# Performance work log

Measured on AMD Instinct MI355X. Metric: run time of the kernel, lower is better.

Reference implementation:

```python
import jax, jax.numpy as jnp
import numpy as np

BS, HW, HIDDEN, TOK, NTOK = 32, 1024, 256, 768, 2048


def setup_inputs() -> dict:
    key = jax.random.key(0)
    ks = jax.random.split(key, 6)
    s = 0.02  # init scale for weights
    return {
        "src": jax.random.normal(ks[0], (HW, BS, HIDDEN), jnp.float32),
        "codebook": jax.random.normal(ks[1], (NTOK, TOK), jnp.float32),
        "w_head": jax.random.normal(ks[2], (TOK, HIDDEN), jnp.float32) * s,
        "w_tail": jax.random.normal(ks[3], (HIDDEN, TOK), jnp.float32) * s,
        "w_pos": jax.random.normal(ks[4], (TOK, TOK), jnp.float32) * s,
        "b_pos": jnp.zeros((TOK,), jnp.float32),
        "w_gate": jax.random.normal(ks[5], (2, 2 * TOK), jnp.float32) * s,
        "h": 32,
        "w": 32,
    }


def reference(src, codebook, w_head, w_tail, w_pos, b_pos, w_gate, h, w):
    N, bs, hidden = src.shape  # [num_visu_token, bs, hidden_dim]
    tok = codebook.shape[1]
    # permute(1,2,0).view(bs,-1,h,w)
    x = jnp.transpose(src, (1, 2, 0)).reshape(bs, hidden, h, w)
    # conv_head: 1x1 conv, no bias
    xq = jnp.einsum("bchw,oc->bohw", x, w_head)  # [bs, tok, h, w]
    # raw-memory reshape, matches torch .view(-1, token_dim)
    flat = xq.reshape(-1, tok)  # [bs*h*w, tok]
    d = (
        jnp.sum(flat * flat, axis=1, keepdims=True)
        - 2.0 * flat @ codebook.T
        + jnp.sum(codebook * codebook, axis=1)[None, :]
    )
    indices = jnp.argmin(d, axis=1)  # [bs*h*w]
    quantized = codebook[indices]  # gather
    # straight-through estimator
    quantized = flat + jax.lax.stop_gradient(quantized - flat)
    # pos_align linear
    quantized = quantized @ w_pos.T + b_pos
    # view(bs, N, tok).permute(0,2,1).view(bs,-1,h,w)
    emb = jnp.transpose(quantized.reshape(bs, N, tok), (0, 2, 1)).reshape(bs, tok, h, w)
    # gated fusion
    gate_in = jnp.concatenate([emb, xq], axis=1)  # [bs, 2*tok, h, w]
    scores = jax.nn.softmax(jnp.einsum("bchw,oc->bohw", gate_in, w_gate), axis=1)
    fused = emb * scores[:, 0:1] + xq * scores[:, 1:2]
    # conv_tail 1x1, then flatten(2).permute(2,0,1)
    out = jnp.einsum("bchw,oc->bohw", fused, w_tail)  # [bs, hidden, h, w]
    out = jnp.transpose(out.reshape(bs, hidden, -1), (2, 0, 1))  # [h*w, bs, hidden]
    return out, indices
```

## Files before the change

### kernel.cpp

```cpp
#include <hip/hip_runtime.h>
#include <cstdint>

#define BSZ 32
#define NVIS 1024
#define HID 256
#define TOKD 768
#define NCODE 2048
#define NPIX 32768

typedef unsigned short u16;
typedef _Float16 half8 __attribute__((ext_vector_type(8)));
typedef unsigned short ushort8 __attribute__((ext_vector_type(8)));
using f32x4 = __attribute__((ext_vector_type(4))) float;

#define AS1 __attribute__((address_space(1)))
#define AS3 __attribute__((address_space(3)))

__device__ __forceinline__ f32x4 mfmaF16(half8 a, half8 b, f32x4 c) {
  return __builtin_amdgcn_mfma_f32_16x16x32_f16(a, b, c, 0, 0, 0);
}

__device__ __forceinline__ unsigned long long pack_key(float d, int idx) {
  unsigned int b = __float_as_uint(d);
  b = (b & 0x80000000u) ? ~b : (b | 0x80000000u);
  return ((unsigned long long)b << 32) | (unsigned int)idx;
}

__device__ __forceinline__ void split16(float v, u16& h, u16& l) {
  union { _Float16 f; u16 u; } a, b;
  a.f = (_Float16)v;
  float hf = (float)a.f;
  b.f = (_Float16)(v - hf);
  h = a.u; l = b.u;
}

__global__ __launch_bounds__(256)
void prep1(const float* __restrict__ cb, const float* __restrict__ wh,
           const float* __restrict__ wt, const float* __restrict__ wp,
           const float* __restrict__ wg, const float* __restrict__ bp,
           u16* __restrict__ cbh, u16* __restrict__ cbl,
           u16* __restrict__ whh, u16* __restrict__ whl,
           float* __restrict__ cbn, float* __restrict__ Mm, float* __restrict__ uv,
           float* __restrict__ Gt, float* __restrict__ g2,
           float* __restrict__ ct0, float* __restrict__ cg) {
  const int bid = blockIdx.x, tid = threadIdx.x;
  if (bid < 6144) {
    int i = bid*256 + tid;
    u16 h, l; split16(cb[i], h, l);
    cbh[i] = h; cbl[i] = l;
  } else if (bid < 6912) {
    int i = (bid - 6144)*256 + tid;
    u16 h, l; split16(wh[i], h, l);
    whh[i] = h; whl[i] = l;
  } else if (bid < 7424) {
    int n = (bid - 6912)*4 + (tid >> 6);
    int lane = tid & 63;
    float a = 0.f;
#pragma unroll
    for (int i = 0; i < 12; ++i) { float v = cb[(long)n*TOKD + lane + 64*i]; a += v*v; }
#pragma unroll
    for (int off = 32; off; off >>= 1) a += __shfl_down(a, off);
    if (lane == 0) cbn[n] = a;
  } else if (bid < 7680) {
    int c2 = bid - 7424, c1 = tid;
    float acc = 0.f;
    for (int t = 0; t < TOKD; ++t) acc += wh[t*HID + c1] * wt[(long)c2*TOKD + t];
    Mm[c1*HID + c2] = acc;
  } else if (bid < 7682) {
    int o = bid - 7680, c1 = tid;
    float acc = 0.f;
    for (int t = 0; t < TOKD; ++t) acc += wh[t*HID + c1] * wg[o*(2*TOKD) + TOKD + t];
    uv[o*HID + c1] = acc;
  } else if (bid < 8450) {
    int rbid = bid - 7682;
    int c = rbid & 255, part = rbid >> 8;
    int tp = part*256 + tid;
    float acc = 0.f;
    for (int t = 0; t < TOKD; ++t) acc += wt[(long)c*TOKD + t] * wp[(long)t*TOKD + tp];
    Gt[(long)tp*HID + c] = acc;
  } else if (bid < 8453) {
    int tp = (bid - 8450)*256 + tid;
    float a0 = 0.f, a1 = 0.f;
    for (int t = 0; t < TOKD; ++t) {
      float wv = wp[(long)t*TOKD + tp];
      a0 += wv * wg[t];
      a1 += wv * wg[2*TOKD + t];
    }
    g2[tp] = a0; g2[TOKD + tp] = a1;
  } else if (bid < 8454) {
    int c = tid;
    float a = 0.f;
    for (int t = 0; t < TOKD; ++t) a += bp[t] * wt[(long)c*TOKD + t];
    ct0[c] = a;
  } else {
    int o = tid >> 6, lane = tid & 63;
    if (o < 2) {
      float a = 0.f;
      for (int t = lane; t < TOKD; t += 64) a += bp[t] * wg[o*(2*TOKD) + t];
#pragma unroll
      for (int off = 32; off; off >>= 1) a += __shfl_down(a, off);
      if (lane == 0) cg[o] = a;
    }
  }
}

__global__ __launch_bounds__(256)
void prep2(const float* __restrict__ cb, const float* __restrict__ Gt,
           const float* __restrict__ ct0, const float* __restrict__ g2,
           const float* __restrict__ cg, float* __restrict__ tc,
           float* __restrict__ gA) {
  __shared__ float cbs[8][TOKD];
  const int n0 = blockIdx.x * 8, tid = threadIdx.x;
  for (int i = tid; i < 8*TOKD; i += 256) cbs[i / TOKD][i % TOKD] = cb[(long)n0*TOKD + i];
  __syncthreads();
  float acc[8] = {};
  for (int t = 0; t < TOKD; ++t) {
    float gv = Gt[(long)t*HID + tid];
#pragma unroll
    for (int i = 0; i < 8; ++i) acc[i] += cbs[i][t] * gv;
  }
  float c0v = ct0[tid];
#pragma unroll
  for (int i = 0; i < 8; ++i) tc[(long)(n0+i)*HID + tid] = acc[i] + c0v;
  {
    int i = tid >> 5, l32 = tid & 31;
    float a0 = 0.f, a1 = 0.f;
    for (int t = l32; t < TOKD; t += 32) {
      float cv = cbs[i][t];
      a0 += cv * g2[t];
      a1 += cv * g2[TOKD + t];
    }
#pragma unroll
    for (int off = 16; off; off >>= 1) { a0 += __shfl_down(a0, off); a1 += __shfl_down(a1, off); }
    if (l32 == 0) { gA[n0+i] = a0 + cg[0]; gA[NCODE + n0+i] = a1 + cg[1]; }
  }
}

__global__ __launch_bounds__(256)
void head_mfma(const u16* __restrict__ whh, const u16* __restrict__ whl,
               const float* __restrict__ src,
               u16* __restrict__ xqh, u16* __restrict__ xql) {
  __shared__ u16 SM[32768] __attribute__((aligned(16)));
  u16* Ah = SM;
  u16* Al = SM + 8192;
  u16* Bh = SM + 16384;
  u16* Bl = SM + 24576;
  const int tid = threadIdx.x, lane = tid & 63, w = tid >> 6;
  const int n = lane & 15, q = lane >> 4;
  const int rh = w & 1, ch = w >> 1;
  const int obase = blockIdx.x * 128, pbase = blockIdx.y * 128, b = blockIdx.z;

  auto stageA = [&](int kc, int buf) {
#pragma unroll
    for (int is = 0; is < 2; ++is) {
      int c = is*256 + tid;
      int t = c >> 6, qq = (c >> 4) & 3, nn = c & 15;
      long off = (long)(obase + t*16 + nn)*HID + kc*32 + qq*8;
      __builtin_amdgcn_global_load_lds((AS1 void*)(whh + off),
          (AS3 void*)&Ah[buf*4096 + c*8], 16, 0, 0);
      __builtin_amdgcn_global_load_lds((AS1 void*)(whl + off),
          (AS3 void*)&Al[buf*4096 + c*8], 16, 0, 0);
    }
  };
  auto stageB = [&](int kc, int buf) {
#pragma unroll
    for (int is = 0; is < 2; ++is) {
      int c = is*256 + tid;
      int t = c >> 6, qq = (c >> 4) & 3, nn = c & 15;
      const float* gp = src + ((long)(pbase + t*16 + nn)*BSZ + b)*HID + kc*32 + qq*8;
      float4 v0 = *(const float4*)gp;
      float4 v1 = *(const float4*)(gp + 4);
      float vv[8] = {v0.x, v0.y, v0.z, v0.w, v1.x, v1.y, v1.z, v1.w};
      ushort8 hv, lv;
#pragma unroll
      for (int j = 0; j < 8; ++j) { u16 hs, ls; split16(vv[j], hs, ls); hv[j] = hs; lv[j] = ls; }
      *(ushort8*)&Bh[buf*4096 + c*8] = hv;
      *(ushort8*)&Bl[buf*4096 + c*8] = lv;
    }
  };

  f32x4 acc[4][4];
#pragma unroll
  for (int i = 0; i < 4; ++i)
#pragma unroll
    for (int j = 0; j < 4; ++j) acc[i][j] = (f32x4){0.f, 0.f, 0.f, 0.f};

  stageA(0, 0); stageB(0, 0);
  __syncthreads();

  for (int kt = 0; kt < HID/32; ++kt) {
    const int buf = kt & 1;
    if (kt + 1 < HID/32) { stageA(kt + 1, buf ^ 1); stageB(kt + 1, buf ^ 1); }
    half8 af[4][2], bf[4][2];
#pragma unroll
    for (int rt = 0; rt < 4; ++rt) {
      int idx = buf*4096 + ((rh*4 + rt)*64 + q*16 + n)*8;
      af[rt][0] = *(const half8*)&Ah[idx];
      af[rt][1] = *(const half8*)&Al[idx];
    }
#pragma unroll
    for (int ct = 0; ct < 4; ++ct) {
      int idx = buf*4096 + ((ch*4 + ct)*64 + q*16 + n)*8;
      bf[ct][0] = *(const half8*)&Bh[idx];
      bf[ct][1] = *(const half8*)&Bl[idx];
    }
#pragma unroll
    for (int rt = 0; rt < 4; ++rt)
#pragma unroll
      for (int ct = 0; ct < 4; ++ct) {
        acc[rt][ct] = mfmaF16(af[rt][0], bf[ct][0], acc[rt][ct]);
        acc[rt][ct] = mfmaF16(af[rt][0], bf[ct][1], acc[rt][ct]);
        acc[rt][ct] = mfmaF16(af[rt][1], bf[ct][0], acc[rt][ct]);
      }
    __syncthreads();
  }

#pragma unroll
  for (int pass = 0; pass < 2; ++pass) {
    u16* dst = pass ? xql : xqh;
#pragma unroll
    for (int rt = 0; rt < 4; ++rt)
#pragma unroll
      for (int ct = 0; ct < 4; ++ct)
#pragma unroll
        for (int reg = 0; reg < 4; ++reg) {
          u16 hs, ls; split16(acc[rt][ct][reg], hs, ls);
          int ol = rh*64 + rt*16 + q*4 + reg;
          int pl = ch*64 + ct*16 + n;
          SM[ol*136 + pl] = pass ? ls : hs;
        }
    __syncthreads();
#pragma unroll
    for (int s = 0; s < 8; ++s) {
      int cc = tid*8 + s;
      int o = cc >> 4, p8 = cc & 15;
      ushort8 v = *(const ushort8*)&SM[o*136 + p8*8];
      *(ushort8*)(dst + ((long)b*TOKD + obase + o)*NVIS + pbase + p8*8) = v;
    }
    __syncthreads();
  }
}

__global__ __launch_bounds__(256)
void retile(u16* __restrict__ bufH, u16* __restrict__ bufL) {
  __shared__ u16 T[96*136] __attribute__((aligned(16)));
  const long tile = blockIdx.x;
  const int tid = threadIdx.x;
#pragma unroll
  for (int pass = 0; pass < 2; ++pass) {
    u16* buf = pass ? bufL : bufH;
    if (pass) __syncthreads();
#pragma unroll
    for (int i = 0; i < 6; ++i) {
      int g = i*256 + tid;
      int row = g / 96, c16 = g % 96;
      ushort8 v = *(const ushort8*)(buf + tile*12288 + row*768 + c16*8);
      *(ushort8*)&T[c16*136 + row*8] = v;
    }
    __syncthreads();
#pragma unroll
    for (int i = 0; i < 6; ++i) {
      int g = i*256 + tid;
      int kc = g >> 6, lp = g & 63;
      int q = lp >> 4, n = lp & 15;
      ushort8 v = *(const ushort8*)&T[(kc*4 + q)*136 + n*8];
      *(ushort8*)(buf + tile*12288 + (long)kc*512 + lp*8) = v;
    }
  }
}

__global__ __launch_bounds__(512, 2)
void vq_mfma(const u16* __restrict__ xqh, const u16* __restrict__ xql,
             const u16* __restrict__ cbh, const u16* __restrict__ cbl,
             const float* __restrict__ cbn, unsigned long long* __restrict__ keys) {
  __shared__ u16 SM[65536] __attribute__((aligned(16)));
  const int bid = blockIdx.x;
  const int rowBlk = bid >> 3, codeBlk = bid & 7;
  const int rowTile0 = rowBlk * 16, codeTile0 = codeBlk * 16;
  const int tid = threadIdx.x, lane = tid & 63, w = tid >> 6;
  const int n = lane & 15, q = lane >> 4;
  const int wr = w >> 2, wc = w & 3;

  const size_t aOff = (size_t)(rowTile0 + 2*w) * 12288 + lane*8;
  const size_t bOff = (size_t)(codeTile0 + 2*w) * 12288 + lane*8;
  const int ldsChunk = (2*w)*512 + lane*8;

  auto STAGE = [&](int ht, int buf) {
    const int seg = (ht >= 48) ? 2 : ((ht >= 24) ? 1 : 0);
    const int kk = ht - seg * 24;
    const u16* pa = ((seg == 1) ? xql : xqh) + aOff + kk*512;
    const u16* pb = ((seg == 2) ? cbl : cbh) + bOff + kk*512;
    u16* la = &SM[buf*8192 + ldsChunk];
    u16* lb = &SM[32768 + buf*8192 + ldsChunk];
    __builtin_amdgcn_global_load_lds((AS1 void*)pa,           (AS3 void*)la,        16, 0, 0);
    __builtin_amdgcn_global_load_lds((AS1 void*)(pa + 12288), (AS3 void*)(la + 512), 16, 0, 0);
    __builtin_amdgcn_global_load_lds((AS1 void*)pb,           (AS3 void*)lb,        16, 0, 0);
    __builtin_amdgcn_global_load_lds((AS1 void*)(pb + 12288), (AS3 void*)(lb + 512), 16, 0, 0);
  };

  f32x4 acc[8][4];
#pragma unroll
  for (int a = 0; a < 8; ++a)
#pragma unroll
    for (int b2 = 0; b2 < 4; ++b2) acc[a][b2] = (f32x4){0.f, 0.f, 0.f, 0.f};

  STAGE(0, 0); STAGE(1, 1); STAGE(2, 2);

#pragma unroll 4
  for (int ht = 0; ht < 72; ++ht) {
    const int pf = (ht + 3 > 71) ? 71 : ht + 3;
    STAGE(pf, (ht + 3) & 3);
    asm volatile("s_waitcnt vmcnt(12)" ::: "memory");
    asm volatile("s_barrier" ::: "memory");
    const int abase = (ht & 3)*8192 + (wr*8)*512 + lane*8;
    const int bbase = 32768 + (ht & 3)*8192 + (wc*4)*512 + lane*8;
    half8 Af[8], Bf[4];
#pragma unroll
    for (int rt = 0; rt < 8; ++rt) Af[rt] = *(const half8*)&SM[abase + rt*512];
#pragma unroll
    for (int ct = 0; ct < 4; ++ct) Bf[ct] = *(const half8*)&SM[bbase + ct*512];
    asm volatile("s_waitcnt lgkmcnt(0)" ::: "memory");
    asm volatile("s_barrier" ::: "memory");
    __builtin_amdgcn_s_setprio(1);
#pragma unroll
    for (int rt = 0; rt < 8; ++rt)
#pragma unroll
      for (int ct = 0; ct < 4; ++ct)
        acc[rt][ct] = mfmaF16(Af[rt], Bf[ct], acc[rt][ct]);
    __builtin_amdgcn_s_setprio(0);
  }

  float cbv[4];
#pragma unroll
  for (int ct = 0; ct < 4; ++ct) cbv[ct] = cbn[(codeTile0 + wc*4 + ct)*16 + n];
#pragma unroll
  for (int rt = 0; rt < 8; ++rt) {
#pragma unroll
    for (int reg = 0; reg < 4; ++reg) {
      float bd = 3.4e38f; int bi = 0;
#pragma unroll
      for (int ct = 0; ct < 4; ++ct) {
        float d = cbv[ct] - 2.0f * acc[rt][ct][reg];
        int code = (codeTile0 + wc*4 + ct)*16 + n;
        if (d < bd) { bd = d; bi = code; }
      }
      unsigned long long k = pack_key(bd, bi);
      unsigned long long v;
      v = __shfl_xor(k, 1); k = (v < k) ? v : k;
      v = __shfl_xor(k, 2); k = (v < k) ? v : k;
      v = __shfl_xor(k, 4); k = (v < k) ? v : k;
      v = __shfl_xor(k, 8); k = (v < k) ? v : k;
      if (n == 0) {
        int row = (rowTile0 + wr*8 + rt)*16 + q*4 + reg;
        atomicMin(&keys[row], k);
      }
    }
  }
}

__global__ __launch_bounds__(256)
void fuse_out(const float* __restrict__ src, const unsigned long long* __restrict__ keys,
              const float* __restrict__ gA, const float* __restrict__ uvec,
              const float* __restrict__ Mm, const float* __restrict__ tailcode,
              float* __restrict__ out, float* __restrict__ outIdx) {
  __shared__ float ss[32][257];
  __shared__ float s0s[32];
  __shared__ int ids[32];
  const int tid = threadIdx.x;
  const int rb = blockIdx.x * 32;
  const int b = rb >> 10;
  const int p0 = rb & 1023;
#pragma unroll
  for (int qq = 0; qq < 32; ++qq)
    ss[qq][tid] = src[(long)(p0 + qq) * (BSZ*HID) + b*HID + tid];
  if (tid < 32) {
    unsigned long long u = keys[rb + tid];
    int id = (int)(unsigned int)(u & 0xFFFFFFFFull);
    ids[tid] = id;
    outIdx[rb + tid] = (float)id;
  }
  __syncthreads();
  {
    const int wv = tid >> 6, lane = tid & 63;
    for (int qq = 0; qq < 8; ++qq) {
      int qp = wv*8 + qq;
      float a0 = 0.f, a1 = 0.f;
#pragma unroll
      for (int i = 0; i < 4; ++i) {
        float v = ss[qp][lane + 64*i];
        a0 += v * uvec[lane + 64*i];
        a1 += v * uvec[HID + lane + 64*i];
      }
#pragma unroll
      for (int off = 32; off; off >>= 1) { a0 += __shfl_down(a0, off); a1 += __shfl_down(a1, off); }
      if (lane == 0) {
        int id = ids[qp];
        float l0 = gA[id] + a0;
        float l1 = gA[NCODE + id] + a1;
        s0s[qp] = 1.0f / (1.0f + expf(l1 - l0));
      }
    }
  }
  __syncthreads();
  const int qg = tid >> 5, cg = tid & 31;
  const int q0 = qg * 4, c0 = cg * 8;
  float acc[4][8] = {};
  for (int cp = 0; cp < HID; ++cp) {
    float4 m0 = *(const float4*)(Mm + cp*HID + c0);
    float4 m1 = *(const float4*)(Mm + cp*HID + c0 + 4);
    float mm[8] = {m0.x,m0.y,m0.z,m0.w,m1.x,m1.y,m1.z,m1.w};
#pragma unroll
    for (int i = 0; i < 4; ++i) {
      float sv = ss[q0+i][cp];
#pragma unroll
      for (int j = 0; j < 8; ++j) acc[i][j] += sv * mm[j];
    }
  }
#pragma unroll
  for (int i = 0; i < 4; ++i) {
    int qp = q0 + i;
    int id = ids[qp];
    float s0 = s0s[qp], s1 = 1.0f - s0;
    const float* tc = tailcode + (long)id*HID + c0;
    float* op = out + (long)(p0+qp)*(BSZ*HID) + b*HID + c0;
    float4 o0, o1;
    o0.x = s0*tc[0] + s1*acc[i][0]; o0.y = s0*tc[1] + s1*acc[i][1];
    o0.z = s0*tc[2] + s1*acc[i][2]; o0.w = s0*tc[3] + s1*acc[i][3];
    o1.x = s0*tc[4] + s1*acc[i][4]; o1.y = s0*tc[5] + s1*acc[i][5];
    o1.z = s0*tc[6] + s1*acc[i][6]; o1.w = s0*tc[7] + s1*acc[i][7];
    *(float4*)(op) = o0; *(float4*)(op+4) = o1;
  }
}

extern "C" void kernel_launch(void* const* d_in, const int* in_sizes, int n_in,
                              void* d_out, int out_size, void* d_ws, size_t ws_size,
                              hipStream_t stream) {
  const float* src    = (const float*)d_in[0];
  const float* cb     = (const float*)d_in[1];
  const float* w_head = (const float*)d_in[2];
  const float* w_tail = (const float*)d_in[3];
  const float* w_pos  = (const float*)d_in[4];
  const float* b_pos  = (const float*)d_in[5];
  const float* w_gate = (const float*)d_in[6];
  float* out = (float*)d_out;

  char* wsp = (char*)d_ws;
  size_t off = 0;
  auto alloc = [&](size_t bytes) {
    off = (off + 255) & ~(size_t)255;
    void* p = wsp + off; off += bytes; return p;
  };
  u16* xqh = (u16*)alloc((size_t)BSZ*TOKD*NVIS*2);
  u16* xql = (u16*)alloc((size_t)BSZ*TOKD*NVIS*2);
  u16* cbh = (u16*)alloc((size_t)NCODE*TOKD*2);
  u16* cbl = (u16*)alloc((size_t)NCODE*TOKD*2);
  u16* whh = (u16*)alloc((size_t)TOKD*HID*2);
  u16* whl = (u16*)alloc((size_t)TOKD*HID*2);
  float* cbn      = (float*)alloc((size_t)NCODE*4);
  float* Gt       = (float*)alloc((size_t)TOKD*HID*4);
  float* g2       = (float*)alloc((size_t)2*TOKD*4);
  float* ct0      = (float*)alloc((size_t)HID*4);
  float* cg       = (float*)alloc((size_t)2*4);
  float* tailcode = (float*)alloc((size_t)NCODE*HID*4);
  float* gA       = (float*)alloc((size_t)2*NCODE*4);
  float* Mm       = (float*)alloc((size_t)HID*HID*4);
  float* uvec     = (float*)alloc((size_t)2*HID*4);
  unsigned long long* keys = (unsigned long long*)alloc((size_t)NPIX*8);
  (void)ws_size; (void)in_sizes; (void)n_in; (void)out_size;

  prep1<<<8455, 256, 0, stream>>>(cb, w_head, w_tail, w_pos, w_gate, b_pos,
                                  cbh, cbl, whh, whl, cbn, Mm, uvec, Gt, g2, ct0, cg);
  retile<<<NCODE/16, 256, 0, stream>>>(cbh, cbl);
  prep2<<<NCODE/8, 256, 0, stream>>>(cb, Gt, ct0, g2, cg, tailcode, gA);

  head_mfma<<<dim3(TOKD/128, NVIS/128, BSZ), 256, 0, stream>>>(whh, whl, src, xqh, xql);
  retile<<<NPIX/16, 256, 0, stream>>>(xqh, xql);

  hipMemsetAsync(keys, 0xFF, (size_t)NPIX*8, stream);
  vq_mfma<<<1024, 512, 0, stream>>>(xqh, xql, cbh, cbl, cbn, keys);

  fuse_out<<<NPIX/32, 256, 0, stream>>>(src, keys, gA, uvec, Mm, tailcode,
                                        out, out + (size_t)NVIS*BSZ*HID);
}
```

Measured before the change: 667.2 us.

## Double-buffer LDS fragment reads in VQ MFMA loop and remap blocks per XCD

Restructures the VQ distance GEMM main loop so the LDS-to-register reads for the next k-step run while the MFMAs of the current step execute, using two ping-pong register fragment sets. The loop is manually unrolled by two with a peeled tail. The block index is also remapped so each XCD works on a contiguous range of row tiles, aiming for better L2 reuse of the activation tiles. This costs more VGPRs for the extra fragments, which may hurt occupancy at launch bounds of 512 threads and 2 blocks. The wait counts and barriers were retuned to match the new schedule.

Measured after the change: 710.3 us. 6.5% more time.

```diff
diff --git a/kernel.cpp b/kernel.cpp
--- a/kernel.cpp
+++ b/kernel.cpp
@@ -275,7 +275,9 @@
              const float* __restrict__ cbn, unsigned long long* __restrict__ keys) {
   __shared__ u16 SM[65536] __attribute__((aligned(16)));
   const int bid = blockIdx.x;
-  const int rowBlk = bid >> 3, codeBlk = bid & 7;
+  const int xcd = bid & 7, slot = bid >> 3;
+  const int rowBlk = xcd * 16 + (slot >> 3);
+  const int codeBlk = slot & 7;
   const int rowTile0 = rowBlk * 16, codeTile0 = codeBlk * 16;
   const int tid = threadIdx.x, lane = tid & 63, w = tid >> 6;
   const int n = lane & 15, q = lane >> 4;
@@ -304,31 +306,55 @@
 #pragma unroll
     for (int b2 = 0; b2 < 4; ++b2) acc[a][b2] = (f32x4){0.f, 0.f, 0.f, 0.f};
 
+  half8 F0A[8], F0B[4], F1A[8], F1B[4];
+
   STAGE(0, 0); STAGE(1, 1); STAGE(2, 2);
-
-#pragma unroll 4
-  for (int ht = 0; ht < 72; ++ht) {
-    const int pf = (ht + 3 > 71) ? 71 : ht + 3;
-    STAGE(pf, (ht + 3) & 3);
-    asm volatile("s_waitcnt vmcnt(12)" ::: "memory");
-    asm volatile("s_barrier" ::: "memory");
-    const int abase = (ht & 3)*8192 + (wr*8)*512 + lane*8;
-    const int bbase = 32768 + (ht & 3)*8192 + (wc*4)*512 + lane*8;
-    half8 Af[8], Bf[4];
-#pragma unroll
-    for (int rt = 0; rt < 8; ++rt) Af[rt] = *(const half8*)&SM[abase + rt*512];
-#pragma unroll
-    for (int ct = 0; ct < 4; ++ct) Bf[ct] = *(const half8*)&SM[bbase + ct*512];
-    asm volatile("s_waitcnt lgkmcnt(0)" ::: "memory");
-    asm volatile("s_barrier" ::: "memory");
-    __builtin_amdgcn_s_setprio(1);
-#pragma unroll
-    for (int rt = 0; rt < 8; ++rt)
-#pragma unroll
-      for (int ct = 0; ct < 4; ++ct)
-        acc[rt][ct] = mfmaF16(Af[rt], Bf[ct], acc[rt][ct]);
-    __builtin_amdgcn_s_setprio(0);
-  }
+  asm volatile("s_waitcnt vmcnt(8)" ::: "memory");
+  asm volatile("s_barrier" ::: "memory");
+  {
+    const int ab = (wr*8)*512 + lane*8;
+    const int bb = 32768 + (wc*4)*512 + lane*8;
+#pragma unroll
+    for (int rt = 0; rt < 8; ++rt) F0A[rt] = *(const half8*)&SM[ab + rt*512];
+#pragma unroll
+    for (int ct = 0; ct < 4; ++ct) F0B[ct] = *(const half8*)&SM[bb + ct*512];
+  }
+
+#define VQ_ITER(HT, CA, CB, NA, NB, DO_READ)                               \
+  {                                                                        \
+    const int ht_ = (HT);                                                  \
+    const int pf_ = (ht_ + 3 > 71) ? 71 : ht_ + 3;                         \
+    STAGE(pf_, (ht_ + 3) & 3);                                             \
+    asm volatile("s_waitcnt vmcnt(8)" ::: "memory");                       \
+    asm volatile("s_barrier" ::: "memory");                                \
+    if (DO_READ) {                                                         \
+      const int b1_ = (ht_ + 1) & 3;                                       \
+      const int ab_ = b1_*8192 + (wr*8)*512 + lane*8;                      \
+      const int bb_ = 32768 + b1_*8192 + (wc*4)*512 + lane*8;              \
+      _Pragma("unroll")                                                    \
+      for (int rt = 0; rt < 8; ++rt) NA[rt] = *(const half8*)&SM[ab_ + rt*512]; \
+      _Pragma("unroll")                                                    \
+      for (int ct = 0; ct < 4; ++ct) NB[ct] = *(const half8*)&SM[bb_ + ct*512]; \
+    }                                                                      \
+    __builtin_amdgcn_s_setprio(1);                                         \
+    _Pragma("unroll")                                                      \
+    for (int rt = 0; rt < 8; ++rt)                                         \
+      _Pragma("unroll")                                                    \
+      for (int ct = 0; ct < 4; ++ct)                                       \
+        acc[rt][ct] = mfmaF16(CA[rt], CB[ct], acc[rt][ct]);                \
+    __builtin_amdgcn_s_setprio(0);                                         \
+    asm volatile("s_waitcnt lgkmcnt(0)" ::: "memory");                     \
+    asm volatile("s_barrier" ::: "memory");                                \
+  }
+
+#pragma unroll 1
+  for (int h2 = 0; h2 < 35; ++h2) {
+    VQ_ITER(2*h2,     F0A, F0B, F1A, F1B, 1);
+    VQ_ITER(2*h2 + 1, F1A, F1B, F0A, F0B, 1);
+  }
+  VQ_ITER(70, F0A, F0B, F1A, F1B, 1);
+  VQ_ITER(71, F1A, F1B, F0A, F0B, 0);
+#undef VQ_ITER
 
   float cbv[4];
 #pragma unroll
```

## Shrink VQ GEMM tile to 256x128 with XCD-aware mapping and double buffering

Applied to the files above, without the earlier changes.

The VQ distance kernel moves from 512-thread blocks covering 256 rows by 256 codes to 256-thread blocks covering 256 rows by 128 codes, doubling the grid. Block IDs are remapped so each XCD handles a contiguous range of row blocks, which should improve L2 reuse of the A tiles. The 4-stage asynchronous prefetch pipeline with manual waitcnt and barriers is replaced by a simple 2-buffer scheme using __syncthreads, and LDS use drops from 128 KB to 48 KB. This may raise occupancy, but it loses deep prefetch and makes the codebook loads less reusable per row tile. The stage-ahead load may not be awaited before the barrier.

Result: slower. 707.3 us (+6.0%).

```diff
diff --git a/kernel.cpp b/kernel.cpp
--- a/kernel.cpp
+++ b/kernel.cpp
@@ -269,33 +269,39 @@
   }
 }
 
-__global__ __launch_bounds__(512, 2)
+__global__ __launch_bounds__(256, 2)
 void vq_mfma(const u16* __restrict__ xqh, const u16* __restrict__ xql,
              const u16* __restrict__ cbh, const u16* __restrict__ cbl,
              const float* __restrict__ cbn, unsigned long long* __restrict__ keys) {
-  __shared__ u16 SM[65536] __attribute__((aligned(16)));
+  __shared__ u16 SM[24576] __attribute__((aligned(16)));
   const int bid = blockIdx.x;
-  const int rowBlk = bid >> 3, codeBlk = bid & 7;
-  const int rowTile0 = rowBlk * 16, codeTile0 = codeBlk * 16;
+  const int xcd = bid & 7, slot = bid >> 3;
+  const int rowBlk = xcd * 16 + (slot >> 4);
+  const int codeBlk = slot & 15;
+  const int rowTile0 = rowBlk * 16;
+  const int codeTile0 = codeBlk * 8;
   const int tid = threadIdx.x, lane = tid & 63, w = tid >> 6;
   const int n = lane & 15, q = lane >> 4;
-  const int wr = w >> 2, wc = w & 3;
-
-  const size_t aOff = (size_t)(rowTile0 + 2*w) * 12288 + lane*8;
+  const int wr = w >> 1, wc = w & 1;
+
+  const size_t aOff = (size_t)(rowTile0 + 4*w) * 12288 + lane*8;
   const size_t bOff = (size_t)(codeTile0 + 2*w) * 12288 + lane*8;
-  const int ldsChunk = (2*w)*512 + lane*8;
+  const int aChunk = (4*w)*512 + lane*8;
+  const int bChunk = (2*w)*512 + lane*8;
 
   auto STAGE = [&](int ht, int buf) {
     const int seg = (ht >= 48) ? 2 : ((ht >= 24) ? 1 : 0);
     const int kk = ht - seg * 24;
     const u16* pa = ((seg == 1) ? xql : xqh) + aOff + kk*512;
     const u16* pb = ((seg == 2) ? cbl : cbh) + bOff + kk*512;
-    u16* la = &SM[buf*8192 + ldsChunk];
-    u16* lb = &SM[32768 + buf*8192 + ldsChunk];
-    __builtin_amdgcn_global_load_lds((AS1 void*)pa,           (AS3 void*)la,        16, 0, 0);
-    __builtin_amdgcn_global_load_lds((AS1 void*)(pa + 12288), (AS3 void*)(la + 512), 16, 0, 0);
-    __builtin_amdgcn_global_load_lds((AS1 void*)pb,           (AS3 void*)lb,        16, 0, 0);
-    __builtin_amdgcn_global_load_lds((AS1 void*)(pb + 12288), (AS3 void*)(lb + 512), 16, 0, 0);
+    u16* la = &SM[buf*8192 + aChunk];
+    u16* lb = &SM[16384 + buf*4096 + bChunk];
+    __builtin_amdgcn_global_load_lds((AS1 void*)pa,             (AS3 void*)la,          16, 0, 0);
+    __builtin_amdgcn_global_load_lds((AS1 void*)(pa + 12288),   (AS3 void*)(la + 512),  16, 0, 0);
+    __builtin_amdgcn_global_load_lds((AS1 void*)(pa + 2*12288), (AS3 void*)(la + 1024), 16, 0, 0);
+    __builtin_amdgcn_global_load_lds((AS1 void*)(pa + 3*12288), (AS3 void*)(la + 1536), 16, 0, 0);
+    __builtin_amdgcn_global_load_lds((AS1 void*)pb,             (AS3 void*)lb,          16, 0, 0);
+    __builtin_amdgcn_global_load_lds((AS1 void*)(pb + 12288),   (AS3 void*)(lb + 512),  16, 0, 0);
   };
 
   f32x4 acc[8][4];
@@ -304,23 +310,20 @@
 #pragma unroll
     for (int b2 = 0; b2 < 4; ++b2) acc[a][b2] = (f32x4){0.f, 0.f, 0.f, 0.f};
 
-  STAGE(0, 0); STAGE(1, 1); STAGE(2, 2);
-
-#pragma unroll 4
+  STAGE(0, 0);
+  __syncthreads();
+
+#pragma unroll 1
   for (int ht = 0; ht < 72; ++ht) {
-    const int pf = (ht + 3 > 71) ? 71 : ht + 3;
-    STAGE(pf, (ht + 3) & 3);
-    asm volatile("s_waitcnt vmcnt(12)" ::: "memory");
-    asm volatile("s_barrier" ::: "memory");
-    const int abase = (ht & 3)*8192 + (wr*8)*512 + lane*8;
-    const int bbase = 32768 + (ht & 3)*8192 + (wc*4)*512 + lane*8;
+    const int buf = ht & 1;
+    if (ht < 71) STAGE(ht + 1, buf ^ 1);
     half8 Af[8], Bf[4];
-#pragma unroll
-    for (int rt = 0; rt < 8; ++rt) Af[rt] = *(const half8*)&SM[abase + rt*512];
-#pragma unroll
-    for (int ct = 0; ct < 4; ++ct) Bf[ct] = *(const half8*)&SM[bbase + ct*512];
-    asm volatile("s_waitcnt lgkmcnt(0)" ::: "memory");
-    asm volatile("s_barrier" ::: "memory");
+    const int ab = buf*8192 + (wr*8)*512 + lane*8;
+    const int bb = 16384 + buf*4096 + (wc*4)*512 + lane*8;
+#pragma unroll
+    for (int rt = 0; rt < 8; ++rt) Af[rt] = *(const half8*)&SM[ab + rt*512];
+#pragma unroll
+    for (int ct = 0; ct < 4; ++ct) Bf[ct] = *(const half8*)&SM[bb + ct*512];
     __builtin_amdgcn_s_setprio(1);
 #pragma unroll
     for (int rt = 0; rt < 8; ++rt)
@@ -328,6 +331,7 @@
       for (int ct = 0; ct < 4; ++ct)
         acc[rt][ct] = mfmaF16(Af[rt], Bf[ct], acc[rt][ct]);
     __builtin_amdgcn_s_setprio(0);
+    __syncthreads();
   }
 
   float cbv[4];
@@ -477,7 +481,7 @@
   retile<<<NPIX/16, 256, 0, stream>>>(xqh, xql);
 
   hipMemsetAsync(keys, 0xFF, (size_t)NPIX*8, stream);
-  vq_mfma<<<1024, 512, 0, stream>>>(xqh, xql, cbh, cbl, cbn, keys);
+  vq_mfma<<<2048, 256, 0, stream>>>(xqh, xql, cbh, cbl, cbn, keys);
 
   fuse_out<<<NPIX/32, 256, 0, stream>>>(src, keys, gA, uvec, Mm, tailcode,
                                         out, out + (size_t)NVIS*BSZ*HID);
```
